# Optimization experiments

Measured on AMD Instinct MI355X. Metric: run time of the kernel, lower is better.

The kernel has to match this reference:

```python
import jax, jax.numpy as jnp
import numpy as np

B, S, D, H = 8, 1024, 512, 8  # batch, seq_len, d_model (per-head!), num_heads


def setup_inputs() -> dict:
    key = jax.random.key(0)
    ks = jax.random.split(key, 9)
    q_ip = jax.random.normal(ks[0], (B, S, D), dtype=jnp.float32)
    k_ip = jax.random.normal(ks[1], (B, S, D), dtype=jnp.float32)
    v_ip = jax.random.normal(ks[2], (B, S, D), dtype=jnp.float32)
    # float padding-style mask, 1 => masked out (added as mask * -1e9)
    mask = (jax.random.uniform(ks[3], (B, 1, S, S)) < 0.1).astype(jnp.float32)
    scale = 1.0 / np.sqrt(D)  # lecun_normal-ish init scale
    wq = jax.random.normal(ks[4], (D, D * H), dtype=jnp.float32) * scale
    wk = jax.random.normal(ks[5], (D, D * H), dtype=jnp.float32) * scale
    wv = jax.random.normal(ks[6], (D, D * H), dtype=jnp.float32) * scale
    wo = jax.random.normal(ks[7], (D * H, D), dtype=jnp.float32) * (1.0 / np.sqrt(D * H))
    bq = jnp.zeros((D * H,), jnp.float32)
    bk = jnp.zeros((D * H,), jnp.float32)
    bv = jnp.zeros((D * H,), jnp.float32)
    bo = jnp.zeros((D,), jnp.float32)
    return {"v_ip": v_ip, "k_ip": k_ip, "q_ip": q_ip, "mask": mask,
            "wq": wq, "bq": bq, "wk": wk, "bk": bk, "wv": wv, "bv": bv,
            "wo": wo, "bo": bo}


def _split_heads(x, batch, heads, depth):
    # (B, S, H*D) -> (B, H, S, D)
    return x.reshape(batch, -1, heads, depth).transpose(0, 2, 1, 3)


def reference(v_ip, k_ip, q_ip, mask, wq, bq, wk, bk, wv, bv, wo, bo):
    batch = q_ip.shape[0]
    depth = q_ip.shape[-1]          # d_model (= per-head depth in this 'narrow' MHA)
    heads = wq.shape[-1] // depth
    q = _split_heads(q_ip @ wq + bq, batch, heads, depth)  # (B,H,Sq,D)
    k = _split_heads(k_ip @ wk + bk, batch, heads, depth)  # (B,H,Sk,D)
    v = _split_heads(v_ip @ wv + bv, batch, heads, depth)  # (B,H,Sk,D)
    logits = jnp.einsum('bhqd,bhkd->bhqk', q, k) / jnp.sqrt(jnp.float32(depth))
    logits = logits + mask * (-1e9)
    attn = jax.nn.softmax(logits, axis=-1)                  # (B,H,Sq,Sk)
    ctx = jnp.einsum('bhqk,bhkd->bhqd', attn, v)
    ctx = ctx.transpose(0, 2, 1, 3).reshape(batch, -1, heads * depth)
    out = ctx @ wo + bo                                     # (B,Sq,d_model)
    return out, attn
```

## Files before the change

kernel.cpp:

```cpp
#include <hip/hip_runtime.h>
#include <stdint.h>
#include <stddef.h>

typedef _Float16 h16;
typedef __attribute__((ext_vector_type(4))) _Float16 h16x4;
typedef __attribute__((ext_vector_type(8))) _Float16 h16x8;
typedef __attribute__((ext_vector_type(4))) float f32x4;

#define MFMA16(a, b, c) __builtin_amdgcn_mfma_f32_16x16x32_f16((a), (b), (c), 0, 0, 0)

#define NB 8
#define SEQ 1024
#define DEP 512
#define NH 8
#define HD 4096
#define BS 8192

static __device__ __forceinline__ void gload_lds16(const void* g, void* l) {
  __builtin_amdgcn_global_load_lds((__attribute__((address_space(1))) void*)(g),
                                   (__attribute__((address_space(3))) void*)(l),
                                   16, 0, 0);
}

static __device__ __forceinline__ h16 f2h(float f) { return (h16)f; }

__global__ __launch_bounds__(256) void k_conv(const float* __restrict__ in,
                                              h16* __restrict__ out, int n4) {
  int i = blockIdx.x * 256 + threadIdx.x;
  if (i < n4) {
    float4 f = ((const float4*)in)[i];
    h16x4 o = { f2h(f.x), f2h(f.y), f2h(f.z), f2h(f.w) };
    ((h16x4*)out)[i] = o;
  }
}

__global__ __launch_bounds__(256) void k_transpose(const float* __restrict__ in,
                                                   h16* __restrict__ out, int R, int C) {
  __shared__ float t[32][33];
  int c0 = blockIdx.x * 32, r0 = blockIdx.y * 32;
  int tx = threadIdx.x & 31, ty = threadIdx.x >> 5;
  for (int p = 0; p < 4; ++p)
    t[ty + p * 8][tx] = in[(size_t)(r0 + ty + p * 8) * C + c0 + tx];
  __syncthreads();
  for (int p = 0; p < 4; ++p)
    out[(size_t)(c0 + ty + p * 8) * R + r0 + tx] = f2h(t[tx][ty + p * 8]);
}

template <int OUT_MODE>
__global__ __launch_bounds__(256) void k_gemm_nt(const h16* __restrict__ A,
                                                 const h16* __restrict__ Bm,
                                                 const float* __restrict__ bias,
                                                 void* __restrict__ Cout,
                                                 int M, int N, int K, int ldc) {
  __shared__ __align__(16) h16 As[128 * 64];
  __shared__ __align__(16) h16 Bs[128 * 64];
  const int tid = threadIdx.x;
  const int lane = tid & 63;
  const int wave = tid >> 6;
  const int wm = (wave >> 1) * 64;
  const int wn = (wave & 1) * 64;
  const int m0 = blockIdx.x * 128;
  const int n0 = blockIdx.y * 128;

  f32x4 acc[4][4];
  for (int i = 0; i < 4; ++i)
    for (int j = 0; j < 4; ++j) acc[i][j] = (f32x4)0.0f;

  const int lrow = lane >> 3;
  const int lcol = (lane & 7) * 8;
  const int fr = lane & 15, qd = lane >> 4;

  for (int k0 = 0; k0 < K; k0 += 64) {
    __syncthreads();
    for (int i = 0; i < 4; ++i) {
      int g = wave * 4 + i;
      int row = g * 8 + lrow;
      gload_lds16(A + (size_t)(m0 + row) * K + k0 + lcol, As + g * 512);
      gload_lds16(Bm + (size_t)(n0 + row) * K + k0 + lcol, Bs + g * 512);
    }
    __syncthreads();
    for (int kk = 0; kk < 64; kk += 32) {
      h16x8 af[4], bf[4];
      for (int i = 0; i < 4; ++i)
        af[i] = *(const h16x8*)(As + (wm + i * 16 + fr) * 64 + kk + qd * 8);
      for (int j = 0; j < 4; ++j)
        bf[j] = *(const h16x8*)(Bs + (wn + j * 16 + fr) * 64 + kk + qd * 8);
      for (int i = 0; i < 4; ++i)
        for (int j = 0; j < 4; ++j) acc[i][j] = MFMA16(af[i], bf[j], acc[i][j]);
    }
  }

  for (int i = 0; i < 4; ++i) {
    for (int j = 0; j < 4; ++j) {
      int mbase = m0 + wm + i * 16 + qd * 4;
      int ncol = n0 + wn + j * 16 + fr;
      float bv = bias ? bias[ncol] : 0.0f;
      if (OUT_MODE == 0) {
        h16* Cp = (h16*)Cout;
        for (int r = 0; r < 4; ++r)
          Cp[(size_t)(mbase + r) * ldc + ncol] = f2h(acc[i][j][r] + bv);
      } else if (OUT_MODE == 2) {
        float* Cp = (float*)Cout;
        for (int r = 0; r < 4; ++r)
          Cp[(size_t)(mbase + r) * ldc + ncol] = acc[i][j][r] + bv;
      } else {
        h16* Vt = (h16*)Cout;
        int bb = mbase >> 10, ss = mbase & 1023;
        int hh = ncol >> 9, dd = ncol & 511;
        size_t addr = ((size_t)((bb * NH + hh) * DEP + dd)) * SEQ + ss;
        h16x4 pk = { f2h(acc[i][j][0] + bv), f2h(acc[i][j][1] + bv),
                     f2h(acc[i][j][2] + bv), f2h(acc[i][j][3] + bv) };
        *(h16x4*)(Vt + addr) = pk;
      }
    }
  }
}

__global__ __launch_bounds__(512) void k_scores(const h16* __restrict__ Q,
                                                const h16* __restrict__ Km,
                                                const float* __restrict__ mask,
                                                float* __restrict__ attn) {
  __shared__ __align__(16) h16 Qs[32 * 512];
  __shared__ float red[8][32];
  const int tid = threadIdx.x, lane = tid & 63, wave = tid >> 6;
  const int qt = blockIdx.x, hh = blockIdx.y, b = blockIdx.z;
  const int q0 = qt * 32;

  for (int i = 0; i < 4; ++i) {
    int row = i * 8 + wave;
    gload_lds16(Q + (size_t)(b * SEQ + q0 + row) * HD + hh * DEP + lane * 8,
                Qs + row * 512);
  }
  __syncthreads();

  const int fr = lane & 15, qd = lane >> 4;
  const int ncol0 = wave * 128;
  f32x4 acc[2][8];
  for (int i = 0; i < 2; ++i)
    for (int j = 0; j < 8; ++j) acc[i][j] = (f32x4)0.0f;

  for (int kk = 0; kk < 512; kk += 32) {
    h16x8 af0 = *(const h16x8*)(Qs + fr * 512 + kk + qd * 8);
    h16x8 af1 = *(const h16x8*)(Qs + (16 + fr) * 512 + kk + qd * 8);
    for (int j = 0; j < 8; ++j) {
      int n = ncol0 + j * 16 + fr;
      h16x8 bf = *(const h16x8*)(Km + (size_t)(b * SEQ + n) * HD + hh * DEP + kk + qd * 8);
      acc[0][j] = MFMA16(af0, bf, acc[0][j]);
      acc[1][j] = MFMA16(af1, bf, acc[1][j]);
    }
  }

  const float scale = 0.044194173824159216f;
  float rmax[2][4];
  for (int i = 0; i < 2; ++i)
    for (int r = 0; r < 4; ++r) rmax[i][r] = -3.4e38f;
  for (int i = 0; i < 2; ++i)
    for (int j = 0; j < 8; ++j)
      for (int r = 0; r < 4; ++r) {
        int lr = i * 16 + qd * 4 + r;
        int cg = ncol0 + j * 16 + fr;
        float v = acc[i][j][r] * scale +
                  mask[(size_t)(b * SEQ + q0 + lr) * SEQ + cg] * (-1e9f);
        acc[i][j][r] = v;
        rmax[i][r] = fmaxf(rmax[i][r], v);
      }
  for (int i = 0; i < 2; ++i)
    for (int r = 0; r < 4; ++r)
      for (int off = 1; off < 16; off <<= 1)
        rmax[i][r] = fmaxf(rmax[i][r], __shfl_xor(rmax[i][r], off, 64));
  if (fr == 0)
    for (int i = 0; i < 2; ++i)
      for (int r = 0; r < 4; ++r) red[wave][i * 16 + qd * 4 + r] = rmax[i][r];
  __syncthreads();
  float gmax[2][4];
  for (int i = 0; i < 2; ++i)
    for (int r = 0; r < 4; ++r) {
      int lr = i * 16 + qd * 4 + r;
      float m = red[0][lr];
      for (int w = 1; w < 8; ++w) m = fmaxf(m, red[w][lr]);
      gmax[i][r] = m;
    }
  __syncthreads();

  float rsum[2][4] = {{0.f, 0.f, 0.f, 0.f}, {0.f, 0.f, 0.f, 0.f}};
  for (int i = 0; i < 2; ++i)
    for (int j = 0; j < 8; ++j)
      for (int r = 0; r < 4; ++r) {
        float e = __expf(acc[i][j][r] - gmax[i][r]);
        acc[i][j][r] = e;
        rsum[i][r] += e;
      }
  for (int i = 0; i < 2; ++i)
    for (int r = 0; r < 4; ++r)
      for (int off = 1; off < 16; off <<= 1)
        rsum[i][r] += __shfl_xor(rsum[i][r], off, 64);
  if (fr == 0)
    for (int i = 0; i < 2; ++i)
      for (int r = 0; r < 4; ++r) red[wave][i * 16 + qd * 4 + r] = rsum[i][r];
  __syncthreads();

  float* ab = attn + (size_t)(b * NH + hh) * (size_t)(SEQ * SEQ);
  for (int i = 0; i < 2; ++i)
    for (int r = 0; r < 4; ++r) {
      int lr = i * 16 + qd * 4 + r;
      float tot = 0.f;
      for (int w = 0; w < 8; ++w) tot += red[w][lr];
      float inv = 1.0f / tot;
      for (int j = 0; j < 8; ++j)
        ab[(size_t)(q0 + lr) * SEQ + ncol0 + j * 16 + fr] = acc[i][j][r] * inv;
    }
}

__global__ __launch_bounds__(256) void k_gemm_pv(const float* __restrict__ P,
                                                 const h16* __restrict__ Vt,
                                                 h16* __restrict__ ctx) {
  __shared__ __align__(16) h16 As[128 * 64];
  __shared__ __align__(16) h16 Bs[128 * 64];
  const int tid = threadIdx.x, lane = tid & 63, wave = tid >> 6;
  const int wm = (wave >> 1) * 64, wn = (wave & 1) * 64;
  const int m0 = blockIdx.x * 128;
  const int n0 = blockIdx.y * 128;
  const int bh = blockIdx.z;
  const float* Pb = P + (size_t)bh * (size_t)(SEQ * SEQ);
  const h16* Vb = Vt + (size_t)bh * (size_t)(DEP * SEQ);

  f32x4 acc[4][4];
  for (int i = 0; i < 4; ++i)
    for (int j = 0; j < 4; ++j) acc[i][j] = (f32x4)0.0f;

  const int arow = tid >> 1;
  const int acol = (tid & 1) * 32;
  const int lrow = lane >> 3, lcol = (lane & 7) * 8;
  const int fr = lane & 15, qd = lane >> 4;

  for (int k0 = 0; k0 < SEQ; k0 += 64) {
    __syncthreads();
    const float* src = Pb + (size_t)(m0 + arow) * SEQ + k0 + acol;
    for (int u = 0; u < 8; ++u) {
      float4 f = ((const float4*)src)[u];
      h16x4 pk = { f2h(f.x), f2h(f.y), f2h(f.z), f2h(f.w) };
      *(h16x4*)(As + arow * 64 + acol + u * 4) = pk;
    }
    for (int i = 0; i < 4; ++i) {
      int g = wave * 4 + i;
      int row = g * 8 + lrow;
      gload_lds16(Vb + (size_t)(n0 + row) * SEQ + k0 + lcol, Bs + g * 512);
    }
    __syncthreads();
    for (int kk = 0; kk < 64; kk += 32) {
      h16x8 af[4], bf[4];
      for (int i = 0; i < 4; ++i)
        af[i] = *(const h16x8*)(As + (wm + i * 16 + fr) * 64 + kk + qd * 8);
      for (int j = 0; j < 4; ++j)
        bf[j] = *(const h16x8*)(Bs + (wn + j * 16 + fr) * 64 + kk + qd * 8);
      for (int i = 0; i < 4; ++i)
        for (int j = 0; j < 4; ++j) acc[i][j] = MFMA16(af[i], bf[j], acc[i][j]);
    }
  }

  const int bb = bh >> 3, hh = bh & 7;
  for (int i = 0; i < 4; ++i)
    for (int j = 0; j < 4; ++j) {
      int s = m0 + wm + i * 16 + qd * 4;
      int d = n0 + wn + j * 16 + fr;
      for (int r = 0; r < 4; ++r)
        ctx[(size_t)(bb * SEQ + s + r) * HD + hh * DEP + d] = f2h(acc[i][j][r]);
    }
}

extern "C" void kernel_launch(void* const* d_in, const int* in_sizes, int n_in,
                              void* d_out, int out_size, void* d_ws, size_t ws_size,
                              hipStream_t stream) {
  const float* v_ip = (const float*)d_in[0];
  const float* k_ip = (const float*)d_in[1];
  const float* q_ip = (const float*)d_in[2];
  const float* mask = (const float*)d_in[3];
  const float* wq = (const float*)d_in[4];
  const float* bq = (const float*)d_in[5];
  const float* wk = (const float*)d_in[6];
  const float* bk = (const float*)d_in[7];
  const float* wv = (const float*)d_in[8];
  const float* bv = (const float*)d_in[9];
  const float* wo = (const float*)d_in[10];
  const float* bo = (const float*)d_in[11];

  char* ws = (char*)d_ws;
  h16* Qh  = (h16*)(ws + (size_t)0);
  h16* Kh  = (h16*)(ws + (size_t)67108864);
  h16* Vt  = (h16*)(ws + (size_t)134217728);
  h16* xq  = (h16*)(ws + (size_t)201326592);
  h16* xk  = (h16*)(ws + (size_t)209715200);
  h16* xv  = (h16*)(ws + (size_t)218103808);
  h16* WqT = (h16*)(ws + (size_t)226492416);
  h16* WkT = (h16*)(ws + (size_t)230686720);
  h16* WvT = (h16*)(ws + (size_t)234881024);
  h16* WoT = (h16*)(ws + (size_t)239075328);
  h16* ctx = Qh;

  float* out = (float*)d_out;
  float* attn = out + (size_t)BS * DEP;

  k_conv<<<4096, 256, 0, stream>>>(q_ip, xq, 1048576);
  k_conv<<<4096, 256, 0, stream>>>(k_ip, xk, 1048576);
  k_conv<<<4096, 256, 0, stream>>>(v_ip, xv, 1048576);
  k_transpose<<<dim3(128, 16), 256, 0, stream>>>(wq, WqT, 512, 4096);
  k_transpose<<<dim3(128, 16), 256, 0, stream>>>(wk, WkT, 512, 4096);
  k_transpose<<<dim3(128, 16), 256, 0, stream>>>(wv, WvT, 512, 4096);
  k_transpose<<<dim3(16, 128), 256, 0, stream>>>(wo, WoT, 4096, 512);
  k_gemm_nt<0><<<dim3(64, 32), 256, 0, stream>>>(xq, WqT, bq, Qh, 8192, 4096, 512, 4096);
  k_gemm_nt<0><<<dim3(64, 32), 256, 0, stream>>>(xk, WkT, bk, Kh, 8192, 4096, 512, 4096);
  k_gemm_nt<1><<<dim3(64, 32), 256, 0, stream>>>(xv, WvT, bv, Vt, 8192, 4096, 512, 0);
  k_scores<<<dim3(32, 8, 8), 512, 0, stream>>>(Qh, Kh, mask, attn);
  k_gemm_pv<<<dim3(8, 4, 64), 256, 0, stream>>>(attn, Vt, ctx);
  k_gemm_nt<2><<<dim3(64, 4), 256, 0, stream>>>(ctx, WoT, bo, out, 8192, 512, 4096, 512);
}
```

Baseline: 1.189 ms.

## Batch QKV launches, retile scores kernel with LDS-staged K and swap grid order

Merges the three input conversions, weight transposes and QKV projection GEMMs into single launches indexed by blockIdx. The scores kernel now handles 64 query rows per block and stages K chunks through swizzled LDS, replacing direct global fragment loads. This halves how often K is re-read per head and improves load coalescing, at the cost of a large dynamic LDS footprint and one block per CU. GEMM grids are also reordered so the N tile varies fastest, which changes L2 reuse of the A rows.

Result: faster. 1.037 ms (-12.7%).

```diff
diff --git a/kernel.cpp b/kernel.cpp
--- a/kernel.cpp
+++ b/kernel.cpp
@@ -24,14 +24,18 @@
 
 static __device__ __forceinline__ h16 f2h(float f) { return (h16)f; }
 
-__global__ __launch_bounds__(256) void k_conv(const float* __restrict__ in,
-                                              h16* __restrict__ out, int n4) {
+__global__ __launch_bounds__(256) void k_conv3(const float* __restrict__ q,
+                                               const float* __restrict__ k,
+                                               const float* __restrict__ v,
+                                               h16* __restrict__ xq, h16* __restrict__ xk,
+                                               h16* __restrict__ xv) {
+  int z = blockIdx.y;
+  const float* in = z == 0 ? q : (z == 1 ? k : v);
+  h16* out = z == 0 ? xq : (z == 1 ? xk : xv);
   int i = blockIdx.x * 256 + threadIdx.x;
-  if (i < n4) {
-    float4 f = ((const float4*)in)[i];
-    h16x4 o = { f2h(f.x), f2h(f.y), f2h(f.z), f2h(f.w) };
-    ((h16x4*)out)[i] = o;
-  }
+  float4 f = ((const float4*)in)[i];
+  h16x4 o = { f2h(f.x), f2h(f.y), f2h(f.z), f2h(f.w) };
+  ((h16x4*)out)[i] = o;
 }
 
 __global__ __launch_bounds__(256) void k_transpose(const float* __restrict__ in,
@@ -44,6 +48,89 @@
   __syncthreads();
   for (int p = 0; p < 4; ++p)
     out[(size_t)(c0 + ty + p * 8) * R + r0 + tx] = f2h(t[tx][ty + p * 8]);
+}
+
+__global__ __launch_bounds__(256) void k_transpose3(const float* __restrict__ wq,
+                                                    const float* __restrict__ wk,
+                                                    const float* __restrict__ wv,
+                                                    h16* __restrict__ oq, h16* __restrict__ ok,
+                                                    h16* __restrict__ ov) {
+  __shared__ float t[32][33];
+  int z = blockIdx.z;
+  const float* in = z == 0 ? wq : (z == 1 ? wk : wv);
+  h16* out = z == 0 ? oq : (z == 1 ? ok : ov);
+  const int R = 512, C = 4096;
+  int c0 = blockIdx.x * 32, r0 = blockIdx.y * 32;
+  int tx = threadIdx.x & 31, ty = threadIdx.x >> 5;
+  for (int p = 0; p < 4; ++p)
+    t[ty + p * 8][tx] = in[(size_t)(r0 + ty + p * 8) * C + c0 + tx];
+  __syncthreads();
+  for (int p = 0; p < 4; ++p)
+    out[(size_t)(c0 + ty + p * 8) * R + r0 + tx] = f2h(t[tx][ty + p * 8]);
+}
+
+__global__ __launch_bounds__(256) void k_gemm_qkv(
+    const h16* __restrict__ xq, const h16* __restrict__ xk, const h16* __restrict__ xv,
+    const h16* __restrict__ WqT, const h16* __restrict__ WkT, const h16* __restrict__ WvT,
+    const float* __restrict__ bq, const float* __restrict__ bk, const float* __restrict__ bv,
+    h16* __restrict__ Qh, h16* __restrict__ Kh, h16* __restrict__ Vt) {
+  __shared__ __align__(16) h16 As[128 * 64];
+  __shared__ __align__(16) h16 Bs[128 * 64];
+  const int z = blockIdx.z;
+  const h16* A = z == 0 ? xq : (z == 1 ? xk : xv);
+  const h16* Bm = z == 0 ? WqT : (z == 1 ? WkT : WvT);
+  const float* bias = z == 0 ? bq : (z == 1 ? bk : bv);
+  const int K = 512;
+  const int tid = threadIdx.x, lane = tid & 63, wave = tid >> 6;
+  const int wm = (wave >> 1) * 64, wn = (wave & 1) * 64;
+  const int m0 = blockIdx.y * 128;
+  const int n0 = blockIdx.x * 128;
+
+  f32x4 acc[4][4];
+  for (int i = 0; i < 4; ++i)
+    for (int j = 0; j < 4; ++j) acc[i][j] = (f32x4)0.0f;
+
+  const int lrow = lane >> 3, lcol = (lane & 7) * 8;
+  const int fr = lane & 15, qd = lane >> 4;
+
+  for (int k0 = 0; k0 < K; k0 += 64) {
+    __syncthreads();
+    for (int i = 0; i < 4; ++i) {
+      int g = wave * 4 + i;
+      int row = g * 8 + lrow;
+      gload_lds16(A + (size_t)(m0 + row) * K + k0 + lcol, As + g * 512);
+      gload_lds16(Bm + (size_t)(n0 + row) * K + k0 + lcol, Bs + g * 512);
+    }
+    __syncthreads();
+    for (int kk = 0; kk < 64; kk += 32) {
+      h16x8 af[4], bf[4];
+      for (int i = 0; i < 4; ++i)
+        af[i] = *(const h16x8*)(As + (wm + i * 16 + fr) * 64 + kk + qd * 8);
+      for (int j = 0; j < 4; ++j)
+        bf[j] = *(const h16x8*)(Bs + (wn + j * 16 + fr) * 64 + kk + qd * 8);
+      for (int i = 0; i < 4; ++i)
+        for (int j = 0; j < 4; ++j) acc[i][j] = MFMA16(af[i], bf[j], acc[i][j]);
+    }
+  }
+
+  h16* Cnat = z == 0 ? Qh : Kh;
+  for (int i = 0; i < 4; ++i)
+    for (int j = 0; j < 4; ++j) {
+      int mbase = m0 + wm + i * 16 + qd * 4;
+      int ncol = n0 + wn + j * 16 + fr;
+      float bv2 = bias[ncol];
+      if (z < 2) {
+        for (int r = 0; r < 4; ++r)
+          Cnat[(size_t)(mbase + r) * HD + ncol] = f2h(acc[i][j][r] + bv2);
+      } else {
+        int bb = mbase >> 10, ss = mbase & 1023;
+        int hh = ncol >> 9, dd = ncol & 511;
+        size_t addr = ((size_t)((bb * NH + hh) * DEP + dd)) * SEQ + ss;
+        h16x4 pk = { f2h(acc[i][j][0] + bv2), f2h(acc[i][j][1] + bv2),
+                     f2h(acc[i][j][2] + bv2), f2h(acc[i][j][3] + bv2) };
+        *(h16x4*)(Vt + addr) = pk;
+      }
+    }
 }
 
 template <int OUT_MODE>
@@ -54,20 +141,16 @@
                                                  int M, int N, int K, int ldc) {
   __shared__ __align__(16) h16 As[128 * 64];
   __shared__ __align__(16) h16 Bs[128 * 64];
-  const int tid = threadIdx.x;
-  const int lane = tid & 63;
-  const int wave = tid >> 6;
-  const int wm = (wave >> 1) * 64;
-  const int wn = (wave & 1) * 64;
-  const int m0 = blockIdx.x * 128;
-  const int n0 = blockIdx.y * 128;
+  const int tid = threadIdx.x, lane = tid & 63, wave = tid >> 6;
+  const int wm = (wave >> 1) * 64, wn = (wave & 1) * 64;
+  const int m0 = blockIdx.y * 128;
+  const int n0 = blockIdx.x * 128;
 
   f32x4 acc[4][4];
   for (int i = 0; i < 4; ++i)
     for (int j = 0; j < 4; ++j) acc[i][j] = (f32x4)0.0f;
 
-  const int lrow = lane >> 3;
-  const int lcol = (lane & 7) * 8;
+  const int lrow = lane >> 3, lcol = (lane & 7) * 8;
   const int fr = lane & 15, qd = lane >> 4;
 
   for (int k0 = 0; k0 < K; k0 += 64) {
@@ -90,71 +173,78 @@
     }
   }
 
-  for (int i = 0; i < 4; ++i) {
+  for (int i = 0; i < 4; ++i)
     for (int j = 0; j < 4; ++j) {
       int mbase = m0 + wm + i * 16 + qd * 4;
       int ncol = n0 + wn + j * 16 + fr;
-      float bv = bias ? bias[ncol] : 0.0f;
-      if (OUT_MODE == 0) {
-        h16* Cp = (h16*)Cout;
-        for (int r = 0; r < 4; ++r)
-          Cp[(size_t)(mbase + r) * ldc + ncol] = f2h(acc[i][j][r] + bv);
-      } else if (OUT_MODE == 2) {
-        float* Cp = (float*)Cout;
-        for (int r = 0; r < 4; ++r)
-          Cp[(size_t)(mbase + r) * ldc + ncol] = acc[i][j][r] + bv;
-      } else {
-        h16* Vt = (h16*)Cout;
-        int bb = mbase >> 10, ss = mbase & 1023;
-        int hh = ncol >> 9, dd = ncol & 511;
-        size_t addr = ((size_t)((bb * NH + hh) * DEP + dd)) * SEQ + ss;
-        h16x4 pk = { f2h(acc[i][j][0] + bv), f2h(acc[i][j][1] + bv),
-                     f2h(acc[i][j][2] + bv), f2h(acc[i][j][3] + bv) };
-        *(h16x4*)(Vt + addr) = pk;
-      }
-    }
-  }
-}
-
-__global__ __launch_bounds__(512) void k_scores(const h16* __restrict__ Q,
-                                                const h16* __restrict__ Km,
-                                                const float* __restrict__ mask,
-                                                float* __restrict__ attn) {
-  __shared__ __align__(16) h16 Qs[32 * 512];
-  __shared__ float red[8][32];
+      float bv2 = bias ? bias[ncol] : 0.0f;
+      float* Cp = (float*)Cout;
+      for (int r = 0; r < 4; ++r)
+        Cp[(size_t)(mbase + r) * ldc + ncol] = acc[i][j][r] + bv2;
+    }
+}
+
+#define TQ 64
+#define QS_LD 520
+#define SMEM_SCORES (TQ * QS_LD * 2 + 1024 * 32 * 2 + 8 * TQ * 4)
+
+__global__ __launch_bounds__(512, 1) void k_scores(const h16* __restrict__ Q,
+                                                   const h16* __restrict__ Km,
+                                                   const float* __restrict__ mask,
+                                                   float* __restrict__ attn) {
+  extern __shared__ __align__(16) char smem[];
+  h16* Qs = (h16*)smem;
+  h16* Ks = (h16*)(smem + TQ * QS_LD * 2);
+  float* red = (float*)(smem + TQ * QS_LD * 2 + 1024 * 32 * 2);
+
   const int tid = threadIdx.x, lane = tid & 63, wave = tid >> 6;
   const int qt = blockIdx.x, hh = blockIdx.y, b = blockIdx.z;
-  const int q0 = qt * 32;
-
-  for (int i = 0; i < 4; ++i) {
-    int row = i * 8 + wave;
-    gload_lds16(Q + (size_t)(b * SEQ + q0 + row) * HD + hh * DEP + lane * 8,
-                Qs + row * 512);
-  }
-  __syncthreads();
-
+  const int q0 = qt * TQ;
   const int fr = lane & 15, qd = lane >> 4;
   const int ncol0 = wave * 128;
-  f32x4 acc[2][8];
-  for (int i = 0; i < 2; ++i)
+
+  {
+    const h16* Qg = Q + (size_t)(b * SEQ + q0) * HD + hh * DEP;
+    for (int it = 0; it < 8; ++it) {
+      int g = tid + it * 512;
+      int row = g >> 6, c8 = g & 63;
+      h16x8 v = *(const h16x8*)(Qg + (size_t)row * HD + c8 * 8);
+      *(h16x8*)(Qs + row * QS_LD + c8 * 8) = v;
+    }
+  }
+
+  f32x4 acc[4][8];
+  for (int i = 0; i < 4; ++i)
     for (int j = 0; j < 8; ++j) acc[i][j] = (f32x4)0.0f;
 
-  for (int kk = 0; kk < 512; kk += 32) {
-    h16x8 af0 = *(const h16x8*)(Qs + fr * 512 + kk + qd * 8);
-    h16x8 af1 = *(const h16x8*)(Qs + (16 + fr) * 512 + kk + qd * 8);
+  for (int kc = 0; kc < 512; kc += 32) {
+    __syncthreads();
+    for (int c = 0; c < 8; ++c) {
+      int nbase = wave * 128 + c * 16;
+      int n = nbase + (lane >> 2);
+      int s = lane & 3;
+      int sp = (s - (n >> 1)) & 3;
+      gload_lds16(Km + (size_t)(b * SEQ + n) * HD + hh * DEP + kc + sp * 8,
+                  Ks + nbase * 32);
+    }
+    __syncthreads();
+    h16x8 af[4];
+    for (int i = 0; i < 4; ++i)
+      af[i] = *(const h16x8*)(Qs + (i * 16 + fr) * QS_LD + kc + qd * 8);
+#pragma unroll
     for (int j = 0; j < 8; ++j) {
       int n = ncol0 + j * 16 + fr;
-      h16x8 bf = *(const h16x8*)(Km + (size_t)(b * SEQ + n) * HD + hh * DEP + kk + qd * 8);
-      acc[0][j] = MFMA16(af0, bf, acc[0][j]);
-      acc[1][j] = MFMA16(af1, bf, acc[1][j]);
+      int slot = (qd + (n >> 1)) & 3;
+      h16x8 bf = *(const h16x8*)(Ks + n * 32 + slot * 8);
+      for (int i = 0; i < 4; ++i) acc[i][j] = MFMA16(af[i], bf, acc[i][j]);
     }
   }
 
   const float scale = 0.044194173824159216f;
-  float rmax[2][4];
-  for (int i = 0; i < 2; ++i)
+  float rmax[4][4];
+  for (int i = 0; i < 4; ++i)
     for (int r = 0; r < 4; ++r) rmax[i][r] = -3.4e38f;
-  for (int i = 0; i < 2; ++i)
+  for (int i = 0; i < 4; ++i)
     for (int j = 0; j < 8; ++j)
       for (int r = 0; r < 4; ++r) {
         int lr = i * 16 + qd * 4 + r;
@@ -164,47 +254,50 @@
         acc[i][j][r] = v;
         rmax[i][r] = fmaxf(rmax[i][r], v);
       }
-  for (int i = 0; i < 2; ++i)
+  for (int i = 0; i < 4; ++i)
     for (int r = 0; r < 4; ++r)
       for (int off = 1; off < 16; off <<= 1)
         rmax[i][r] = fmaxf(rmax[i][r], __shfl_xor(rmax[i][r], off, 64));
+  __syncthreads();
   if (fr == 0)
-    for (int i = 0; i < 2; ++i)
-      for (int r = 0; r < 4; ++r) red[wave][i * 16 + qd * 4 + r] = rmax[i][r];
-  __syncthreads();
-  float gmax[2][4];
-  for (int i = 0; i < 2; ++i)
+    for (int i = 0; i < 4; ++i)
+      for (int r = 0; r < 4; ++r) red[wave * TQ + i * 16 + qd * 4 + r] = rmax[i][r];
+  __syncthreads();
+  float gmax[4][4];
+  for (int i = 0; i < 4; ++i)
     for (int r = 0; r < 4; ++r) {
       int lr = i * 16 + qd * 4 + r;
-      float m = red[0][lr];
-      for (int w = 1; w < 8; ++w) m = fmaxf(m, red[w][lr]);
+      float m = red[lr];
+      for (int w = 1; w < 8; ++w) m = fmaxf(m, red[w * TQ + lr]);
       gmax[i][r] = m;
     }
   __syncthreads();
 
-  float rsum[2][4] = {{0.f, 0.f, 0.f, 0.f}, {0.f, 0.f, 0.f, 0.f}};
-  for (int i = 0; i < 2; ++i)
+  float rsum[4][4];
+  for (int i = 0; i < 4; ++i)
+    for (int r = 0; r < 4; ++r) rsum[i][r] = 0.f;
+  for (int i = 0; i < 4; ++i)
     for (int j = 0; j < 8; ++j)
       for (int r = 0; r < 4; ++r) {
         float e = __expf(acc[i][j][r] - gmax[i][r]);
         acc[i][j][r] = e;
         rsum[i][r] += e;
       }
-  for (int i = 0; i < 2; ++i)
+  for (int i = 0; i < 4; ++i)
     for (int r = 0; r < 4; ++r)
       for (int off = 1; off < 16; off <<= 1)
         rsum[i][r] += __shfl_xor(rsum[i][r], off, 64);
   if (fr == 0)
-    for (int i = 0; i < 2; ++i)
-      for (int r = 0; r < 4; ++r) red[wave][i * 16 + qd * 4 + r] = rsum[i][r];
+    for (int i = 0; i < 4; ++i)
+      for (int r = 0; r < 4; ++r) red[wave * TQ + i * 16 + qd * 4 + r] = rsum[i][r];
   __syncthreads();
 
   float* ab = attn + (size_t)(b * NH + hh) * (size_t)(SEQ * SEQ);
-  for (int i = 0; i < 2; ++i)
+  for (int i = 0; i < 4; ++i)
     for (int r = 0; r < 4; ++r) {
       int lr = i * 16 + qd * 4 + r;
       float tot = 0.f;
-      for (int w = 0; w < 8; ++w) tot += red[w][lr];
+      for (int w = 0; w < 8; ++w) tot += red[w * TQ + lr];
       float inv = 1.0f / tot;
       for (int j = 0; j < 8; ++j)
         ab[(size_t)(q0 + lr) * SEQ + ncol0 + j * 16 + fr] = acc[i][j][r] * inv;
@@ -218,8 +311,8 @@
   __shared__ __align__(16) h16 Bs[128 * 64];
   const int tid = threadIdx.x, lane = tid & 63, wave = tid >> 6;
   const int wm = (wave >> 1) * 64, wn = (wave & 1) * 64;
-  const int m0 = blockIdx.x * 128;
-  const int n0 = blockIdx.y * 128;
+  const int m0 = blockIdx.y * 128;
+  const int n0 = blockIdx.x * 128;
   const int bh = blockIdx.z;
   const float* Pb = P + (size_t)bh * (size_t)(SEQ * SEQ);
   const h16* Vb = Vt + (size_t)bh * (size_t)(DEP * SEQ);
@@ -300,17 +393,15 @@
   float* out = (float*)d_out;
   float* attn = out + (size_t)BS * DEP;
 
-  k_conv<<<4096, 256, 0, stream>>>(q_ip, xq, 1048576);
-  k_conv<<<4096, 256, 0, stream>>>(k_ip, xk, 1048576);
-  k_conv<<<4096, 256, 0, stream>>>(v_ip, xv, 1048576);
-  k_transpose<<<dim3(128, 16), 256, 0, stream>>>(wq, WqT, 512, 4096);
-  k_transpose<<<dim3(128, 16), 256, 0, stream>>>(wk, WkT, 512, 4096);
-  k_transpose<<<dim3(128, 16), 256, 0, stream>>>(wv, WvT, 512, 4096);
+  hipFuncSetAttribute((const void*)k_scores,
+                      hipFuncAttributeMaxDynamicSharedMemorySize, SMEM_SCORES);
+
+  k_conv3<<<dim3(4096, 3), 256, 0, stream>>>(q_ip, k_ip, v_ip, xq, xk, xv);
+  k_transpose3<<<dim3(128, 16, 3), 256, 0, stream>>>(wq, wk, wv, WqT, WkT, WvT);
   k_transpose<<<dim3(16, 128), 256, 0, stream>>>(wo, WoT, 4096, 512);
-  k_gemm_nt<0><<<dim3(64, 32), 256, 0, stream>>>(xq, WqT, bq, Qh, 8192, 4096, 512, 4096);
-  k_gemm_nt<0><<<dim3(64, 32), 256, 0, stream>>>(xk, WkT, bk, Kh, 8192, 4096, 512, 4096);
-  k_gemm_nt<1><<<dim3(64, 32), 256, 0, stream>>>(xv, WvT, bv, Vt, 8192, 4096, 512, 0);
-  k_scores<<<dim3(32, 8, 8), 512, 0, stream>>>(Qh, Kh, mask, attn);
-  k_gemm_pv<<<dim3(8, 4, 64), 256, 0, stream>>>(attn, Vt, ctx);
-  k_gemm_nt<2><<<dim3(64, 4), 256, 0, stream>>>(ctx, WoT, bo, out, 8192, 512, 4096, 512);
-}
+  k_gemm_qkv<<<dim3(32, 64, 3), 256, 0, stream>>>(xq, xk, xv, WqT, WkT, WvT,
+                                                  bq, bk, bv, Qh, Kh, Vt);
+  k_scores<<<dim3(SEQ / TQ, NH, NB), 512, SMEM_SCORES, stream>>>(Qh, Kh, mask, attn);
+  k_gemm_pv<<<dim3(4, 8, 64), 256, 0, stream>>>(attn, Vt, ctx);
+  k_gemm_nt<2><<<dim3(4, 64), 256, 0, stream>>>(ctx, WoT, bo, out, 8192, 512, 4096, 512);
+}
```
